# Performance work log

Measured on AMD Instinct MI355X. Metric: run time of the kernel, lower is better.

The kernel has to match this reference:

```python
import jax, jax.numpy as jnp
import numpy as np

N_HEAD, D_K, D_V, D_MODEL = 16, 64, 64, 1024
B, S = 2, 2048


def setup_inputs() -> dict:
    key = jax.random.key(0)
    ks = jax.random.split(key, 9)
    Q = jax.random.normal(ks[0], (B, S, D_MODEL), jnp.float32)
    K = jax.random.normal(ks[1], (B, S, D_MODEL), jnp.float32)
    V = jax.random.normal(ks[2], (B, S, D_MODEL), jnp.float32)
    mask = jax.random.randint(ks[3], (B, 1, S), 0, 2) > 0  # bool, ~half valid
    # xavier-normal-ish std for (d_model, d_k) fan
    std_qk = (2.0 / (D_MODEL + D_K)) ** 0.5
    std_v = (2.0 / (D_MODEL + D_V)) ** 0.5
    Wq = std_qk * jax.random.normal(ks[4], (N_HEAD, D_MODEL, D_K), jnp.float32)
    Wk = std_qk * jax.random.normal(ks[5], (N_HEAD, D_MODEL, D_K), jnp.float32)
    Wv = std_v * jax.random.normal(ks[6], (N_HEAD, D_MODEL, D_V), jnp.float32)
    bound = (6.0 / (N_HEAD * D_V)) ** 0.5  # kaiming_uniform-ish
    Wo = jax.random.uniform(ks[7], (N_HEAD * D_V, D_MODEL), jnp.float32, -bound, bound)
    return {"Q": Q, "K": K, "V": V, "Wq": Wq, "Wk": Wk, "Wv": Wv, "Wo": Wo, "mask": mask}


def reference(Q, K, V, Wq, Wk, Wv, Wo, mask):
    n_head, d_model, d_k = Wq.shape
    d_v = Wv.shape[-1]
    b, sq, _ = Q.shape
    sk = K.shape[1]
    # Per-head projections; torch cat over heads == leading head axis here.
    q = jnp.einsum('bsd,hdk->hbsk', Q, Wq)  # (H,B,Sq,dk)
    k = jnp.einsum('bsd,hdk->hbsk', K, Wk)  # (H,B,Sk,dk)
    v = jnp.einsum('bsd,hdv->hbsv', V, Wv)  # (H,B,Sk,dv)
    scores = jnp.einsum('hbqk,hbsk->hbqs', q, k) / (d_k ** 0.5)
    m = mask[None]  # (1,B,1,Sk), broadcasts over heads and queries
    scores = jnp.where(m, scores, -1e9)
    attn = jax.nn.softmax(scores, axis=-1)
    attn = jnp.where(m, attn, 0.0)
    out = jnp.einsum('hbqs,hbsv->hbqv', attn, v)  # (H,B,Sq,dv)
    # torch: split along batch*head dim then cat on feature dim -> head-major feature concat
    out = jnp.transpose(out, (1, 2, 0, 3)).reshape(b, sq, n_head * d_v)
    out = out @ Wo  # (B,Sq,d_model); dropout is identity in eval
    attns = attn.reshape(n_head * b, sq, sk)
    return out, attns
```

## Files before the change

kernel.cpp:

```cpp
#include <hip/hip_runtime.h>
#include <hip/hip_bf16.h>

typedef __attribute__((ext_vector_type(8))) short short8;
typedef __attribute__((ext_vector_type(4))) float floatx4;

#define H 16
#define BB 2
#define SS 2048
#define DM 1024
#define DK 64

__device__ __forceinline__ unsigned short f2bf(float f) {
  union { float f; unsigned int u; } x; x.f = f;
  unsigned int r = (x.u + 0x7fffu + ((x.u >> 16) & 1u)) >> 16;
  return (unsigned short)r;
}
__device__ __forceinline__ float bf2f(unsigned short h) {
  union { unsigned int u; float f; } x; x.u = (unsigned int)h << 16;
  return x.f;
}
__device__ __forceinline__ void gld16(const unsigned short* g, unsigned short* l) {
  __builtin_amdgcn_global_load_lds(
      (const __attribute__((address_space(1))) unsigned int*)(g),
      (__attribute__((address_space(3))) unsigned int*)(l), 16, 0, 0);
}

__global__ __launch_bounds__(256) void convert_qkv(
    const float* __restrict__ Q, const float* __restrict__ K, const float* __restrict__ V,
    unsigned short* __restrict__ Qb, unsigned short* __restrict__ Kb,
    unsigned short* __restrict__ Vb) {
  const float* in; unsigned short* out;
  int z = blockIdx.y;
  if (z == 0)      { in = Q; out = Qb; }
  else if (z == 1) { in = K; out = Kb; }
  else             { in = V; out = Vb; }
  size_t i = ((size_t)blockIdx.x * 256 + threadIdx.x) * 4;
  float4 v = *(const float4*)&in[i];
  ushort4 o;
  o.x = f2bf(v.x); o.y = f2bf(v.y); o.z = f2bf(v.z); o.w = f2bf(v.w);
  *(ushort4*)&out[i] = o;
}

__global__ __launch_bounds__(256) void repack_w(
    const float* __restrict__ Wq, const float* __restrict__ Wk,
    const float* __restrict__ Wv, const float* __restrict__ Wo,
    unsigned short* __restrict__ Wq_t, unsigned short* __restrict__ Wk_t,
    unsigned short* __restrict__ Wv_t, unsigned short* __restrict__ Wo_t) {
  int z = blockIdx.z;
  int bx = blockIdx.x, by = blockIdx.y;
  int t = threadIdx.x;
  const float* in;
  unsigned short* out;
  if (z == 0)      { in = Wq; out = Wq_t; }
  else if (z == 1) { in = Wk; out = Wk_t; }
  else if (z == 2) { in = Wv; out = Wv_t; }
  else             { in = Wo; out = Wo_t; }
  #pragma unroll
  for (int i = 0; i < 16; i++) {
    int o = t + i * 256;
    int r = o >> 6, cloc = o & 63;
    if (z < 3) {
      out[(bx * 64 + r) * 1024 + by * 64 + cloc] =
          f2bf(in[bx * 65536 + (by * 64 + cloc) * 64 + r]);
    } else {
      out[(bx * 64 + r) * 1024 + by * 64 + cloc] =
          f2bf(in[(by * 64 + cloc) * 1024 + bx * 64 + r]);
    }
  }
}

__global__ __launch_bounds__(256) void gemm_bt(
    const unsigned short* __restrict__ A, const unsigned short* __restrict__ Bt,
    unsigned short* __restrict__ C, float* __restrict__ Cf, int M, int N, int K) {
  __shared__ __align__(16) unsigned short a_lds[128 * 64];
  __shared__ __align__(16) unsigned short b_lds[64 * 64];
  const int bn = blockIdx.x * 64, bm = blockIdx.y * 128;
  const int t = threadIdx.x;
  const int wave = t >> 6, lane = t & 63;
  const int quad = lane >> 4, l15 = lane & 15;
  const int wm = (wave & 1) * 64, wn = (wave >> 1) * 32;
  floatx4 acc[4][2] = {};
  for (int kt = 0; kt < K; kt += 64) {
    __syncthreads();
    #pragma unroll
    for (int it = 0; it < 4; it++) {
      int c = t + it * 256;
      int r = c >> 3, ck = c & 7;
      gld16(&A[(size_t)(bm + r) * K + kt + ((ck ^ (r & 7)) * 8)], &a_lds[c * 8]);
    }
    #pragma unroll
    for (int it = 0; it < 2; it++) {
      int c = t + it * 256;
      int r = c >> 3, ck = c & 7;
      gld16(&Bt[(size_t)(bn + r) * K + kt + ((ck ^ (r & 7)) * 8)], &b_lds[c * 8]);
    }
    __syncthreads();
    #pragma unroll
    for (int kk = 0; kk < 2; kk++) {
      short8 af[4], bfr[2];
      #pragma unroll
      for (int mt = 0; mt < 4; mt++) {
        int r = wm + mt * 16 + l15;
        af[mt] = *(const short8*)&a_lds[r * 64 + (((kk * 4 + quad) ^ (r & 7)) * 8)];
      }
      #pragma unroll
      for (int nt = 0; nt < 2; nt++) {
        int r = wn + nt * 16 + l15;
        bfr[nt] = *(const short8*)&b_lds[r * 64 + (((kk * 4 + quad) ^ (r & 7)) * 8)];
      }
      #pragma unroll
      for (int mt = 0; mt < 4; mt++)
        #pragma unroll
        for (int nt = 0; nt < 2; nt++)
          acc[mt][nt] = __builtin_amdgcn_mfma_f32_16x16x32_bf16(af[mt], bfr[nt], acc[mt][nt], 0, 0, 0);
    }
  }
  if (Cf) {
    #pragma unroll
    for (int mt = 0; mt < 4; mt++)
      #pragma unroll
      for (int nt = 0; nt < 2; nt++)
        #pragma unroll
        for (int r = 0; r < 4; r++) {
          int row = bm + wm + mt * 16 + quad * 4 + r;
          int col = bn + wn + nt * 16 + l15;
          Cf[(size_t)row * N + col] = acc[mt][nt][r];
        }
  } else {
    #pragma unroll
    for (int mt = 0; mt < 4; mt++)
      #pragma unroll
      for (int nt = 0; nt < 2; nt++)
        #pragma unroll
        for (int r = 0; r < 4; r++) {
          int row = bm + wm + mt * 16 + quad * 4 + r;
          int col = bn + wn + nt * 16 + l15;
          C[(size_t)row * N + col] = f2bf(acc[mt][nt][r]);
        }
  }
}

__global__ __launch_bounds__(256) void attn_kernel(
    const unsigned short* __restrict__ q2, const unsigned short* __restrict__ k2,
    const unsigned short* __restrict__ vt, const void* __restrict__ mask,
    float* __restrict__ attns, unsigned short* __restrict__ ctx) {
  __shared__ __align__(16) unsigned short k_lds[128 * 72];
  __shared__ __align__(16) unsigned short vt_lds[64 * 136];
  __shared__ unsigned char masku8[SS];
  __shared__ float rowsum_inv[64];
  __shared__ int s_fp32, s_byte2, s_gt1;
  const int qt = blockIdx.x, b = blockIdx.y, h = blockIdx.z;
  const int t = threadIdx.x;
  const int wave = t >> 6, lane = t & 63;
  const int quad = lane >> 4, l15 = lane & 15;

  if (t == 0) { s_fp32 = 1; s_byte2 = 0; s_gt1 = 0; }
  __syncthreads();
  {
    const unsigned int* mw = (const unsigned int*)mask;
    int f_fp32 = 1, f_byte2 = 0, f_gt1 = 0;
    for (int i = t; i < 1024; i += 256) {
      unsigned int w = mw[i];
      if (!(w == 0u || w == 0x3F800000u)) f_fp32 = 0;
      if (((w & 0xFFu) > 1u) || (((w >> 8) & 0xFFu) > 1u) ||
          (((w >> 16) & 0xFFu) > 1u) || ((w >> 24) > 1u)) f_byte2 = 1;
      if (w > 1u) f_gt1 = 1;
    }
    if (!f_fp32) atomicAnd(&s_fp32, 0);
    if (f_byte2) atomicOr(&s_byte2, 1);
    if (f_gt1)  atomicOr(&s_gt1, 1);
  }
  __syncthreads();
  {
    const unsigned int*   mw = (const unsigned int*)mask;
    const unsigned short* mh = (const unsigned short*)mask;
    const unsigned char*  mb = (const unsigned char*)mask;
    int mode = s_fp32 ? 0 : (s_byte2 ? 1 : (s_gt1 ? 2 : 3));
    for (int i = t; i < SS; i += 256) {
      int idx = b * SS + i;
      bool mv;
      if (mode == 0)      mv = mw[idx] != 0u;
      else if (mode == 1) mv = mh[idx] != 0u;
      else if (mode == 2) mv = mb[idx] != 0u;
      else                mv = mw[idx] != 0u;
      masku8[i] = mv ? 1 : 0;
    }
  }

  {
    int c = t;
    #pragma unroll
    for (int it = 0; it < 2; it++, c += 256) {
      int r = c >> 3, cc = (c & 7) * 8;
      *(uint4*)&k_lds[r * 72 + cc] =
          *(const uint4*)&q2[(size_t)(b * SS + qt * 64 + r) * DM + h * DK + cc];
    }
  }
  __syncthreads();
  short8 aq0 = *(const short8*)&k_lds[(wave * 16 + l15) * 72 + quad * 8];
  short8 aq1 = *(const short8*)&k_lds[(wave * 16 + l15) * 72 + 32 + quad * 8];

  const float cexp = 0.18033688011112042f;
  float rs[4] = {0.f, 0.f, 0.f, 0.f};

  for (int kt = 0; kt < 16; kt++) {
    __syncthreads();
    {
      int c = t;
      #pragma unroll
      for (int it = 0; it < 4; it++, c += 256) {
        int r = c >> 3, cc = (c & 7) * 8;
        *(uint4*)&k_lds[r * 72 + cc] =
            *(const uint4*)&k2[(size_t)(b * SS + kt * 128 + r) * DM + h * DK + cc];
      }
    }
    __syncthreads();
    #pragma unroll
    for (int ct = 0; ct < 8; ct++) {
      floatx4 s = {};
      short8 bk0 = *(const short8*)&k_lds[(ct * 16 + l15) * 72 + quad * 8];
      short8 bk1 = *(const short8*)&k_lds[(ct * 16 + l15) * 72 + 32 + quad * 8];
      s = __builtin_amdgcn_mfma_f32_16x16x32_bf16(aq0, bk0, s, 0, 0, 0);
      s = __builtin_amdgcn_mfma_f32_16x16x32_bf16(aq1, bk1, s, 0, 0, 0);
      float m = (float)masku8[kt * 128 + ct * 16 + l15];
      #pragma unroll
      for (int r = 0; r < 4; r++) rs[r] += m * exp2f(s[r] * cexp);
    }
  }
  #pragma unroll
  for (int r = 0; r < 4; r++) {
    rs[r] += __shfl_xor(rs[r], 1);
    rs[r] += __shfl_xor(rs[r], 2);
    rs[r] += __shfl_xor(rs[r], 4);
    rs[r] += __shfl_xor(rs[r], 8);
  }
  if (l15 == 0) {
    #pragma unroll
    for (int r = 0; r < 4; r++)
      rowsum_inv[wave * 16 + quad * 4 + r] = rs[r] > 0.f ? 1.0f / rs[r] : 0.f;
  }
  __syncthreads();
  float rinv[4];
  #pragma unroll
  for (int r = 0; r < 4; r++) rinv[r] = rowsum_inv[wave * 16 + quad * 4 + r];

  floatx4 cacc[4] = {};
  const size_t attn_base = ((size_t)(h * BB + b) * SS + qt * 64) * SS;

  for (int kt = 0; kt < 16; kt++) {
    __syncthreads();
    {
      int c = t;
      #pragma unroll
      for (int it = 0; it < 4; it++, c += 256) {
        int r = c >> 3, cc = (c & 7) * 8;
        *(uint4*)&k_lds[r * 72 + cc] =
            *(const uint4*)&k2[(size_t)(b * SS + kt * 128 + r) * DM + h * DK + cc];
      }
      c = t;
      #pragma unroll
      for (int it = 0; it < 4; it++, c += 256) {
        int n = c >> 4, cc = (c & 15) * 8;
        *(uint4*)&vt_lds[n * 136 + cc] =
            *(const uint4*)&vt[(size_t)(h * DK + n) * (BB * SS) + b * SS + kt * 128 + cc];
      }
    }
    __syncthreads();
    floatx4 sv[8];
    #pragma unroll
    for (int ct = 0; ct < 8; ct++) {
      floatx4 s = {};
      short8 bk0 = *(const short8*)&k_lds[(ct * 16 + l15) * 72 + quad * 8];
      short8 bk1 = *(const short8*)&k_lds[(ct * 16 + l15) * 72 + 32 + quad * 8];
      s = __builtin_amdgcn_mfma_f32_16x16x32_bf16(aq0, bk0, s, 0, 0, 0);
      sv[ct] = __builtin_amdgcn_mfma_f32_16x16x32_bf16(aq1, bk1, s, 0, 0, 0);
    }
    __syncthreads();
    #pragma unroll
    for (int ct = 0; ct < 8; ct++) {
      float m = (float)masku8[kt * 128 + ct * 16 + l15];
      #pragma unroll
      for (int r = 0; r < 4; r++) {
        float p = m * exp2f(sv[ct][r] * cexp) * rinv[r];
        k_lds[(wave * 16 + quad * 4 + r) * 136 + ct * 16 + l15] = f2bf(p);
      }
    }
    __syncthreads();
    {
      int c = t;
      #pragma unroll
      for (int it = 0; it < 8; it++, c += 256) {
        int r = c >> 5, fc = (c & 31) * 4;
        ushort4 u = *(const ushort4*)&k_lds[r * 136 + fc];
        float4 f;
        f.x = bf2f(u.x); f.y = bf2f(u.y);
        f.z = bf2f(u.z); f.w = bf2f(u.w);
        *(float4*)&attns[attn_base + (size_t)r * SS + kt * 128 + fc] = f;
      }
    }
    #pragma unroll
    for (int ks = 0; ks < 4; ks++) {
      short8 ap = *(const short8*)&k_lds[(wave * 16 + l15) * 136 + ks * 32 + quad * 8];
      #pragma unroll
      for (int ct = 0; ct < 4; ct++) {
        short8 bv = *(const short8*)&vt_lds[(ct * 16 + l15) * 136 + ks * 32 + quad * 8];
        cacc[ct] = __builtin_amdgcn_mfma_f32_16x16x32_bf16(ap, bv, cacc[ct], 0, 0, 0);
      }
    }
  }
  #pragma unroll
  for (int ct = 0; ct < 4; ct++)
    #pragma unroll
    for (int r = 0; r < 4; r++) {
      int row = b * SS + qt * 64 + wave * 16 + quad * 4 + r;
      int col = h * DK + ct * 16 + l15;
      ctx[(size_t)row * DM + col] = f2bf(cacc[ct][r]);
    }
}

extern "C" void kernel_launch(void* const* d_in, const int* in_sizes, int n_in,
                              void* d_out, int out_size, void* d_ws, size_t ws_size,
                              hipStream_t stream) {
  (void)in_sizes; (void)n_in; (void)out_size; (void)ws_size;
  const float* Q  = (const float*)d_in[0];
  const float* K  = (const float*)d_in[1];
  const float* V  = (const float*)d_in[2];
  const float* Wq = (const float*)d_in[3];
  const float* Wk = (const float*)d_in[4];
  const float* Wv = (const float*)d_in[5];
  const float* Wo = (const float*)d_in[6];
  const void* mask = d_in[7];

  float* out   = (float*)d_out;
  float* attns = out + (size_t)BB * SS * DM;

  char* ws = (char*)d_ws;
  unsigned short* Qb   = (unsigned short*)(ws);
  unsigned short* Kb   = (unsigned short*)(ws + (size_t)(8u  << 20));
  unsigned short* Vb   = (unsigned short*)(ws + (size_t)(16u << 20));
  unsigned short* q2   = (unsigned short*)(ws + (size_t)(24u << 20));
  unsigned short* k2   = (unsigned short*)(ws + (size_t)(32u << 20));
  unsigned short* vt   = (unsigned short*)(ws + (size_t)(40u << 20));
  unsigned short* ctx  = (unsigned short*)(ws + (size_t)(48u << 20));
  unsigned short* Wq_t = (unsigned short*)(ws + (size_t)(56u << 20));
  unsigned short* Wk_t = (unsigned short*)(ws + (size_t)(58u << 20));
  unsigned short* Wv_t = (unsigned short*)(ws + (size_t)(60u << 20));
  unsigned short* Wo_t = (unsigned short*)(ws + (size_t)(62u << 20));

  convert_qkv<<<dim3(4096, 3), 256, 0, stream>>>(Q, K, V, Qb, Kb, Vb);
  repack_w<<<dim3(16, 16, 4), 256, 0, stream>>>(Wq, Wk, Wv, Wo, Wq_t, Wk_t, Wv_t, Wo_t);
  gemm_bt<<<dim3(16, 32), 256, 0, stream>>>(Qb, Wq_t, q2, nullptr, 4096, 1024, 1024);
  gemm_bt<<<dim3(16, 32), 256, 0, stream>>>(Kb, Wk_t, k2, nullptr, 4096, 1024, 1024);
  gemm_bt<<<dim3(64, 8), 256, 0, stream>>>(Wv_t, Vb, vt, nullptr, 1024, 4096, 1024);
  attn_kernel<<<dim3(32, 2, 16), 256, 0, stream>>>(q2, k2, vt, mask, attns, ctx);
  gemm_bt<<<dim3(16, 32), 256, 0, stream>>>(ctx, Wo_t, nullptr, out, 4096, 1024, 1024);
}
```

Measured before the change: 895.1 us.

## Halve attention key tile and pack K, V, P into one LDS buffer

The second attention pass now processes 64 keys per iteration instead of 128. K, V-transpose and the probability tile sit in disjoint regions of a single shared buffer. Because P no longer overwrites the K tile, one barrier per iteration is dropped, and the 8-entry score register array is gone. The intent is lower LDS and VGPR use for higher occupancy, at the cost of twice as many iterations, each with its own barriers and smaller global loads.

```diff
diff --git a/kernel.cpp b/kernel.cpp
--- a/kernel.cpp
+++ b/kernel.cpp
@@ -140,12 +140,13 @@
   }
 }
 
+#define VB (64 * 72)
+#define PB (128 * 72)
 __global__ __launch_bounds__(256) void attn_kernel(
     const unsigned short* __restrict__ q2, const unsigned short* __restrict__ k2,
     const unsigned short* __restrict__ vt, const void* __restrict__ mask,
     float* __restrict__ attns, unsigned short* __restrict__ ctx) {
-  __shared__ __align__(16) unsigned short k_lds[128 * 72];
-  __shared__ __align__(16) unsigned short vt_lds[64 * 136];
+  __shared__ __align__(16) unsigned short buf[192 * 72];
   __shared__ unsigned char masku8[SS];
   __shared__ float rowsum_inv[64];
   __shared__ int s_fp32, s_byte2, s_gt1;
@@ -192,13 +193,13 @@
     #pragma unroll
     for (int it = 0; it < 2; it++, c += 256) {
       int r = c >> 3, cc = (c & 7) * 8;
-      *(uint4*)&k_lds[r * 72 + cc] =
+      *(uint4*)&buf[r * 72 + cc] =
           *(const uint4*)&q2[(size_t)(b * SS + qt * 64 + r) * DM + h * DK + cc];
     }
   }
   __syncthreads();
-  short8 aq0 = *(const short8*)&k_lds[(wave * 16 + l15) * 72 + quad * 8];
-  short8 aq1 = *(const short8*)&k_lds[(wave * 16 + l15) * 72 + 32 + quad * 8];
+  short8 aq0 = *(const short8*)&buf[(wave * 16 + l15) * 72 + quad * 8];
+  short8 aq1 = *(const short8*)&buf[(wave * 16 + l15) * 72 + 32 + quad * 8];
 
   const float cexp = 0.18033688011112042f;
   float rs[4] = {0.f, 0.f, 0.f, 0.f};
@@ -210,7 +211,7 @@
       #pragma unroll
       for (int it = 0; it < 4; it++, c += 256) {
         int r = c >> 3, cc = (c & 7) * 8;
-        *(uint4*)&k_lds[r * 72 + cc] =
+        *(uint4*)&buf[r * 72 + cc] =
             *(const uint4*)&k2[(size_t)(b * SS + kt * 128 + r) * DM + h * DK + cc];
       }
     }
@@ -218,8 +219,8 @@
     #pragma unroll
     for (int ct = 0; ct < 8; ct++) {
       floatx4 s = {};
-      short8 bk0 = *(const short8*)&k_lds[(ct * 16 + l15) * 72 + quad * 8];
-      short8 bk1 = *(const short8*)&k_lds[(ct * 16 + l15) * 72 + 32 + quad * 8];
+      short8 bk0 = *(const short8*)&buf[(ct * 16 + l15) * 72 + quad * 8];
+      short8 bk1 = *(const short8*)&buf[(ct * 16 + l15) * 72 + 32 + quad * 8];
       s = __builtin_amdgcn_mfma_f32_16x16x32_bf16(aq0, bk0, s, 0, 0, 0);
       s = __builtin_amdgcn_mfma_f32_16x16x32_bf16(aq1, bk1, s, 0, 0, 0);
       float m = (float)masku8[kt * 128 + ct * 16 + l15];
@@ -247,63 +248,58 @@
   floatx4 cacc[4] = {};
   const size_t attn_base = ((size_t)(h * BB + b) * SS + qt * 64) * SS;
 
-  for (int kt = 0; kt < 16; kt++) {
+  for (int kt = 0; kt < 32; kt++) {
     __syncthreads();
     {
       int c = t;
       #pragma unroll
-      for (int it = 0; it < 4; it++, c += 256) {
+      for (int it = 0; it < 2; it++, c += 256) {
         int r = c >> 3, cc = (c & 7) * 8;
-        *(uint4*)&k_lds[r * 72 + cc] =
-            *(const uint4*)&k2[(size_t)(b * SS + kt * 128 + r) * DM + h * DK + cc];
+        *(uint4*)&buf[r * 72 + cc] =
+            *(const uint4*)&k2[(size_t)(b * SS + kt * 64 + r) * DM + h * DK + cc];
       }
       c = t;
       #pragma unroll
-      for (int it = 0; it < 4; it++, c += 256) {
-        int n = c >> 4, cc = (c & 15) * 8;
-        *(uint4*)&vt_lds[n * 136 + cc] =
-            *(const uint4*)&vt[(size_t)(h * DK + n) * (BB * SS) + b * SS + kt * 128 + cc];
-      }
-    }
-    __syncthreads();
-    floatx4 sv[8];
-    #pragma unroll
-    for (int ct = 0; ct < 8; ct++) {
+      for (int it = 0; it < 2; it++, c += 256) {
+        int n = c >> 3, cc = (c & 7) * 8;
+        *(uint4*)&buf[VB + n * 72 + cc] =
+            *(const uint4*)&vt[(size_t)(h * DK + n) * (BB * SS) + b * SS + kt * 64 + cc];
+      }
+    }
+    __syncthreads();
+    #pragma unroll
+    for (int ct = 0; ct < 4; ct++) {
       floatx4 s = {};
-      short8 bk0 = *(const short8*)&k_lds[(ct * 16 + l15) * 72 + quad * 8];
-      short8 bk1 = *(const short8*)&k_lds[(ct * 16 + l15) * 72 + 32 + quad * 8];
+      short8 bk0 = *(const short8*)&buf[(ct * 16 + l15) * 72 + quad * 8];
+      short8 bk1 = *(const short8*)&buf[(ct * 16 + l15) * 72 + 32 + quad * 8];
       s = __builtin_amdgcn_mfma_f32_16x16x32_bf16(aq0, bk0, s, 0, 0, 0);
-      sv[ct] = __builtin_amdgcn_mfma_f32_16x16x32_bf16(aq1, bk1, s, 0, 0, 0);
-    }
-    __syncthreads();
-    #pragma unroll
-    for (int ct = 0; ct < 8; ct++) {
-      float m = (float)masku8[kt * 128 + ct * 16 + l15];
+      s = __builtin_amdgcn_mfma_f32_16x16x32_bf16(aq1, bk1, s, 0, 0, 0);
+      float m = (float)masku8[kt * 64 + ct * 16 + l15];
       #pragma unroll
       for (int r = 0; r < 4; r++) {
-        float p = m * exp2f(sv[ct][r] * cexp) * rinv[r];
-        k_lds[(wave * 16 + quad * 4 + r) * 136 + ct * 16 + l15] = f2bf(p);
+        float p = m * exp2f(s[r] * cexp) * rinv[r];
+        buf[PB + (wave * 16 + quad * 4 + r) * 72 + ct * 16 + l15] = f2bf(p);
       }
     }
     __syncthreads();
     {
       int c = t;
       #pragma unroll
-      for (int it = 0; it < 8; it++, c += 256) {
-        int r = c >> 5, fc = (c & 31) * 4;
-        ushort4 u = *(const ushort4*)&k_lds[r * 136 + fc];
+      for (int it = 0; it < 4; it++, c += 256) {
+        int r = c >> 4, fc = (c & 15) * 4;
+        ushort4 u = *(const ushort4*)&buf[PB + r * 72 + fc];
         float4 f;
         f.x = bf2f(u.x); f.y = bf2f(u.y);
         f.z = bf2f(u.z); f.w = bf2f(u.w);
-        *(float4*)&attns[attn_base + (size_t)r * SS + kt * 128 + fc] = f;
-      }
-    }
-    #pragma unroll
-    for (int ks = 0; ks < 4; ks++) {
-      short8 ap = *(const short8*)&k_lds[(wave * 16 + l15) * 136 + ks * 32 + quad * 8];
+        *(float4*)&attns[attn_base + (size_t)r * SS + kt * 64 + fc] = f;
+      }
+    }
+    #pragma unroll
+    for (int ks = 0; ks < 2; ks++) {
+      short8 ap = *(const short8*)&buf[PB + (wave * 16 + l15) * 72 + ks * 32 + quad * 8];
       #pragma unroll
       for (int ct = 0; ct < 4; ct++) {
-        short8 bv = *(const short8*)&vt_lds[(ct * 16 + l15) * 136 + ks * 32 + quad * 8];
+        short8 bv = *(const short8*)&buf[VB + (ct * 16 + l15) * 72 + ks * 32 + quad * 8];
         cacc[ct] = __builtin_amdgcn_mfma_f32_16x16x32_bf16(ap, bv, cacc[ct], 0, 0, 0);
       }
     }
```

New measurement: 782.8 us. 1.14x faster.
